# Optimization experiments

Hardware: AMD Instinct MI355X
Metric: run time of the kernel (lower is better)

## Reference

```python
import jax, jax.numpy as jnp
import numpy as np

D_MODEL = 2048
HIDDEN = 1024
NUM_EXPERTS = 8
TOTAL_TOKENS = 16384  # tokens already sorted/grouped by expert


def setup_inputs() -> dict:
    key = jax.random.key(0)
    k1, k2, k3 = jax.random.split(key, 3)
    x = jax.random.normal(k1, (TOTAL_TOKENS, D_MODEL), dtype=jnp.float32)
    # nn.Linear(d_model, 2*E*H).weight -> [2*E*H, d_model]
    w_up_gate = jax.random.normal(k2, (2 * NUM_EXPERTS * HIDDEN, D_MODEL), dtype=jnp.float32) / np.sqrt(D_MODEL)
    # nn.Linear(E*H, d_model).weight -> [d_model, E*H]
    w_down = jax.random.normal(k3, (D_MODEL, NUM_EXPERTS * HIDDEN), dtype=jnp.float32) / np.sqrt(HIDDEN)
    batch_size_per_expert = jnp.full((NUM_EXPERTS,), TOTAL_TOKENS // NUM_EXPERTS, dtype=jnp.int32)
    return {
        "x": x,
        "w_up_gate": w_up_gate,
        "w_down": w_down,
        "batch_size_per_expert": batch_size_per_expert,
        "num_experts": NUM_EXPERTS,
    }


def reference(x, w_up_gate, w_down, batch_size_per_expert, num_experts):
    # Per-expert sizes are host constants (a Python list in the torch code).
    sizes = np.asarray(batch_size_per_expert)
    offs = np.concatenate([[0], np.cumsum(sizes)])  # static token offsets
    d_model = x.shape[-1]
    hidden = w_up_gate.shape[0] // (2 * num_experts)
    # [E, 2H, d_model]: expert e's fused up/gate weight block
    w_ug = w_up_gate.reshape(num_experts, 2 * hidden, d_model)
    outs = []
    for e in range(num_experts):  # small static loop over experts (ragged grouped GEMM)
        xe = x[offs[e]:offs[e + 1]]                      # [n_e, d_model]
        ug = xe @ w_ug[e].T                              # [n_e, 2H]
        h = jax.nn.silu(ug[:, :hidden]) * ug[:, hidden:]  # SwiGLU, [n_e, H]
        wd_e = w_down[:, e * hidden:(e + 1) * hidden]    # [d_model, H]
        outs.append(h @ wd_e.T)                          # [n_e, d_model]
    return jnp.concatenate(outs, axis=0)
```

## Files before the change

kernel.cpp:

```cpp
#include <hip/hip_runtime.h>
#include <hip/hip_bf16.h>

typedef __attribute__((ext_vector_type(8))) short short8;
typedef __attribute__((ext_vector_type(4))) float float4v;

#define BM 128
#define BK 32
#define LDSK 40

struct alignas(8) BF4 { unsigned short x, y, z, w; };
struct alignas(16) I4 { int x, y, z, w; };

__device__ __forceinline__ unsigned short f2bf(float f) {
    union { float f; unsigned u; } v; v.f = f;
    unsigned u = v.u + (0x7FFFu + ((v.u >> 16) & 1u));
    return (unsigned short)(u >> 16);
}

__device__ __forceinline__ void stage_f32_tile(const float* __restrict__ src, long ld,
                                               unsigned short* lds, int t) {
    const int rr  = t >> 3;
    const int col = (t & 7) << 2;
    #pragma unroll
    for (int r = 0; r < 4; ++r) {
        const int row = rr + r * 32;
        const float4 v = *(const float4*)(src + (long)row * ld + col);
        BF4 o; o.x = f2bf(v.x); o.y = f2bf(v.y); o.z = f2bf(v.z); o.w = f2bf(v.w);
        *(BF4*)(lds + row * LDSK + col) = o;
    }
}

__device__ __forceinline__ int find_expert(const int* __restrict__ bspe, int row0) {
    int e = 0, off = 0;
    #pragma unroll
    for (int i = 0; i < 8; ++i) {
        int s = bspe[i];
        if (row0 < off + s) { e = i; break; }
        off += s;
    }
    return e;
}

__global__ __launch_bounds__(256) void moe_up_gate(
    const float* __restrict__ x, const float* __restrict__ wug,
    const int* __restrict__ bspe, unsigned short* __restrict__ hws) {
    __shared__ alignas(16) unsigned short As[BM * LDSK];
    __shared__ alignas(16) unsigned short Bs[BM * LDSK];

    const int t = threadIdx.x;
    const int lane = t & 63;
    const int w = t >> 6;
    const int wr = w >> 1, wc = w & 1;
    const int bm = blockIdx.y;
    const int h0 = blockIdx.x * 64;
    const int row0 = bm * BM;

    const int e = find_expert(bspe, row0);

    const float* abase = x + (long)row0 * 2048;
    const float* bup = wug + ((long)e * 2048 + h0) * 2048;
    const float* bgt = wug + ((long)e * 2048 + 1024 + h0) * 2048;

    float4v acc[4][4];
    #pragma unroll
    for (int m = 0; m < 4; ++m)
        #pragma unroll
        for (int n = 0; n < 4; ++n)
            acc[m][n] = (float4v){0.f, 0.f, 0.f, 0.f};

    const int k8 = (lane >> 4) << 3;
    const int am = wr * 64 + (lane & 15);
    const int l15 = lane & 15;

    for (int k0 = 0; k0 < 2048; k0 += BK) {
        __syncthreads();
        stage_f32_tile(abase + k0, 2048, As, t);
        {
            const int rr  = t >> 3;
            const int col = (t & 7) << 2;
            #pragma unroll
            for (int r = 0; r < 4; ++r) {
                const int row = rr + r * 32;
                const float* p = (row < 64 ? bup + (long)row * 2048
                                           : bgt + (long)(row - 64) * 2048) + k0 + col;
                const float4 v = *(const float4*)p;
                BF4 o; o.x = f2bf(v.x); o.y = f2bf(v.y); o.z = f2bf(v.z); o.w = f2bf(v.w);
                *(BF4*)(Bs + row * LDSK + col) = o;
            }
        }
        __syncthreads();

        short8 a[4], b[4];
        #pragma unroll
        for (int m = 0; m < 4; ++m)
            a[m] = *(const short8*)(As + (am + m * 16) * LDSK + k8);
        #pragma unroll
        for (int n = 0; n < 4; ++n) {
            const int rb = (n < 2) ? (wc * 32 + n * 16) : (64 + wc * 32 + (n - 2) * 16);
            b[n] = *(const short8*)(Bs + (rb + l15) * LDSK + k8);
        }
        #pragma unroll
        for (int m = 0; m < 4; ++m)
            #pragma unroll
            for (int n = 0; n < 4; ++n)
                acc[m][n] = __builtin_amdgcn_mfma_f32_16x16x32_bf16(a[m], b[n], acc[m][n], 0, 0, 0);
    }

    const int rbase = row0 + wr * 64 + (lane >> 4) * 4;
    const int cbase = h0 + wc * 32 + l15;
    #pragma unroll
    for (int m = 0; m < 4; ++m)
        #pragma unroll
        for (int n = 0; n < 2; ++n)
            #pragma unroll
            for (int q = 0; q < 4; ++q) {
                const float u = acc[m][n][q];
                const float g = acc[m][n + 2][q];
                const float s = u / (1.f + __expf(-u));
                const int row = rbase + m * 16 + q;
                const int col = cbase + n * 16;
                hws[(long)row * 1024 + col] = f2bf(s * g);
            }
}

__global__ __launch_bounds__(256) void moe_down(
    const unsigned short* __restrict__ hws, const float* __restrict__ wd,
    const int* __restrict__ bspe, float* __restrict__ out) {
    __shared__ alignas(16) unsigned short As[BM * LDSK];
    __shared__ alignas(16) unsigned short Bs[BM * LDSK];

    const int t = threadIdx.x;
    const int lane = t & 63;
    const int w = t >> 6;
    const int wr = w >> 1, wc = w & 1;
    const int bm = blockIdx.y;
    const int n0 = blockIdx.x * BM;
    const int row0 = bm * BM;

    const int e = find_expert(bspe, row0);

    const unsigned short* abase = hws + (long)row0 * 1024;
    const float* bbase = wd + (long)n0 * 8192 + e * 1024;

    float4v acc[4][4];
    #pragma unroll
    for (int m = 0; m < 4; ++m)
        #pragma unroll
        for (int n = 0; n < 4; ++n)
            acc[m][n] = (float4v){0.f, 0.f, 0.f, 0.f};

    const int k8 = (lane >> 4) << 3;
    const int am = wr * 64 + (lane & 15);
    const int l15 = lane & 15;

    for (int k0 = 0; k0 < 1024; k0 += BK) {
        __syncthreads();
        {
            const int row = t >> 2;
            const int col = (t & 3) << 3;
            #pragma unroll
            for (int r = 0; r < 2; ++r) {
                const I4 v = *(const I4*)(abase + (long)(row + r * 64) * 1024 + k0 + col);
                *(I4*)(As + (row + r * 64) * LDSK + col) = v;
            }
        }
        stage_f32_tile(bbase + k0, 8192, Bs, t);
        __syncthreads();

        short8 a[4], b[4];
        #pragma unroll
        for (int m = 0; m < 4; ++m)
            a[m] = *(const short8*)(As + (am + m * 16) * LDSK + k8);
        #pragma unroll
        for (int n = 0; n < 4; ++n)
            b[n] = *(const short8*)(Bs + (wc * 64 + n * 16 + l15) * LDSK + k8);
        #pragma unroll
        for (int m = 0; m < 4; ++m)
            #pragma unroll
            for (int n = 0; n < 4; ++n)
                acc[m][n] = __builtin_amdgcn_mfma_f32_16x16x32_bf16(a[m], b[n], acc[m][n], 0, 0, 0);
    }

    const int rbase = row0 + wr * 64 + (lane >> 4) * 4;
    const int cbase = n0 + wc * 64 + l15;
    #pragma unroll
    for (int m = 0; m < 4; ++m)
        #pragma unroll
        for (int n = 0; n < 4; ++n)
            #pragma unroll
            for (int q = 0; q < 4; ++q)
                out[(long)(rbase + m * 16 + q) * 2048 + cbase + n * 16] = acc[m][n][q];
}

extern "C" void kernel_launch(void* const* d_in, const int* in_sizes, int n_in,
                              void* d_out, int out_size, void* d_ws, size_t ws_size,
                              hipStream_t stream) {
    const float* x   = (const float*)d_in[0];
    const float* wug = (const float*)d_in[1];
    const float* wd  = (const float*)d_in[2];
    const int*  bspe = (const int*)d_in[3];
    float* out = (float*)d_out;
    unsigned short* hws = (unsigned short*)d_ws;

    moe_up_gate<<<dim3(16, 128), dim3(256), 0, stream>>>(x, wug, bspe, hws);
    moe_down  <<<dim3(16, 128), dim3(256), 0, stream>>>(hws, wd, bspe, out);
}
```

Measured before the change: 684.3 us.

## Pre-convert inputs to bf16 and stage tiles via direct global-to-LDS loads

Adds a standalone fp32-to-bf16 conversion pass for x, the up/gate weights and the down weights, reusing workspace so the down-weight copy overwrites the no-longer-needed x buffer. New GEMM kernels then read bf16 directly and load tiles into LDS with global_load_lds, removing the per-tile float loads and in-loop conversion from the GEMM main loops. In exchange, every call adds extra full-tensor read/write passes and depends on a large workspace, otherwise it falls back to the old path. The new LDS layout drops the padding, which may introduce bank conflicts.

```diff
diff --git a/kernel.cpp b/kernel.cpp
--- a/kernel.cpp
+++ b/kernel.cpp
@@ -9,12 +9,195 @@
 #define LDSK 40
 
 struct alignas(8) BF4 { unsigned short x, y, z, w; };
+struct alignas(16) BF8 { unsigned short s[8]; };
 struct alignas(16) I4 { int x, y, z, w; };
 
 __device__ __forceinline__ unsigned short f2bf(float f) {
     union { float f; unsigned u; } v; v.f = f;
     unsigned u = v.u + (0x7FFFu + ((v.u >> 16) & 1u));
     return (unsigned short)(u >> 16);
+}
+
+__device__ __forceinline__ int find_expert(const int* __restrict__ bspe, int row0) {
+    int e = 0, off = 0;
+    #pragma unroll
+    for (int i = 0; i < 8; ++i) {
+        int s = bspe[i];
+        if (row0 < off + s) { e = i; break; }
+        off += s;
+    }
+    return e;
+}
+
+__device__ __forceinline__ void gload_lds16(const unsigned short* g, unsigned short* l) {
+    __builtin_amdgcn_global_load_lds(
+        (const __attribute__((address_space(1))) void*)g,
+        (__attribute__((address_space(3))) void*)l, 16, 0, 0);
+}
+
+__global__ __launch_bounds__(256) void f32_to_bf16(const float* __restrict__ src,
+                                                   unsigned short* __restrict__ dst,
+                                                   long n) {
+    const long stride = (long)gridDim.x * 256 * 8;
+    for (long i = ((long)blockIdx.x * 256 + threadIdx.x) * 8; i < n; i += stride) {
+        const float4 v0 = *(const float4*)(src + i);
+        const float4 v1 = *(const float4*)(src + i + 4);
+        BF8 o;
+        o.s[0] = f2bf(v0.x); o.s[1] = f2bf(v0.y); o.s[2] = f2bf(v0.z); o.s[3] = f2bf(v0.w);
+        o.s[4] = f2bf(v1.x); o.s[5] = f2bf(v1.y); o.s[6] = f2bf(v1.z); o.s[7] = f2bf(v1.w);
+        *(BF8*)(dst + i) = o;
+    }
+}
+
+__global__ __launch_bounds__(256) void moe_up_gate_bf(
+    const unsigned short* __restrict__ xb, const unsigned short* __restrict__ wb,
+    const int* __restrict__ bspe, unsigned short* __restrict__ hws) {
+    __shared__ alignas(16) unsigned short As[128 * 32];
+    __shared__ alignas(16) unsigned short Bs[128 * 32];
+
+    const int t = threadIdx.x;
+    const int lane = t & 63;
+    const int w = t >> 6;
+    const int wr = w >> 1, wc = w & 1;
+    const int bm = blockIdx.y;
+    const int h0 = blockIdx.x * 64;
+    const int row0 = bm * BM;
+
+    const int e = find_expert(bspe, row0);
+
+    const unsigned short* abase = xb + (long)row0 * 2048;
+    const unsigned short* bup = wb + ((long)e * 2048 + h0) * 2048;
+    const unsigned short* bgt = wb + ((long)e * 2048 + 1024 + h0) * 2048;
+
+    float4v acc[4][4];
+    #pragma unroll
+    for (int m = 0; m < 4; ++m)
+        #pragma unroll
+        for (int n = 0; n < 4; ++n)
+            acc[m][n] = (float4v){0.f, 0.f, 0.f, 0.f};
+
+    const int j0 = w, j1 = w + 4;
+    const int srow = lane >> 2;
+    const int scol = (lane & 3) << 3;
+    const unsigned short* a0 = abase + (long)(j0 * 16 + srow) * 2048 + scol;
+    const unsigned short* a1 = abase + (long)(j1 * 16 + srow) * 2048 + scol;
+    const unsigned short* b0 = bup + (long)(j0 * 16 + srow) * 2048 + scol;
+    const unsigned short* b1 = bgt + (long)((j1 - 4) * 16 + srow) * 2048 + scol;
+
+    const int k8 = (lane >> 4) << 3;
+    const int am = wr * 64 + (lane & 15);
+    const int l15 = lane & 15;
+
+    for (int k0 = 0; k0 < 2048; k0 += BK) {
+        __syncthreads();
+        gload_lds16(a0 + k0, As + j0 * 512);
+        gload_lds16(a1 + k0, As + j1 * 512);
+        gload_lds16(b0 + k0, Bs + j0 * 512);
+        gload_lds16(b1 + k0, Bs + j1 * 512);
+        __syncthreads();
+
+        short8 a[4], b[4];
+        #pragma unroll
+        for (int m = 0; m < 4; ++m)
+            a[m] = *(const short8*)(As + (am + m * 16) * 32 + k8);
+        #pragma unroll
+        for (int n = 0; n < 4; ++n) {
+            const int rb = (n < 2) ? (wc * 32 + n * 16) : (64 + wc * 32 + (n - 2) * 16);
+            b[n] = *(const short8*)(Bs + (rb + l15) * 32 + k8);
+        }
+        #pragma unroll
+        for (int m = 0; m < 4; ++m)
+            #pragma unroll
+            for (int n = 0; n < 4; ++n)
+                acc[m][n] = __builtin_amdgcn_mfma_f32_16x16x32_bf16(a[m], b[n], acc[m][n], 0, 0, 0);
+    }
+
+    const int rbase = row0 + wr * 64 + (lane >> 4) * 4;
+    const int cbase = h0 + wc * 32 + l15;
+    #pragma unroll
+    for (int m = 0; m < 4; ++m)
+        #pragma unroll
+        for (int n = 0; n < 2; ++n)
+            #pragma unroll
+            for (int q = 0; q < 4; ++q) {
+                const float u = acc[m][n][q];
+                const float g = acc[m][n + 2][q];
+                const float s = u / (1.f + __expf(-u));
+                const int row = rbase + m * 16 + q;
+                const int col = cbase + n * 16;
+                hws[(long)row * 1024 + col] = f2bf(s * g);
+            }
+}
+
+__global__ __launch_bounds__(256) void moe_down_bf(
+    const unsigned short* __restrict__ hws, const unsigned short* __restrict__ wdb,
+    const int* __restrict__ bspe, float* __restrict__ out) {
+    __shared__ alignas(16) unsigned short As[128 * 32];
+    __shared__ alignas(16) unsigned short Bs[128 * 32];
+
+    const int t = threadIdx.x;
+    const int lane = t & 63;
+    const int w = t >> 6;
+    const int wr = w >> 1, wc = w & 1;
+    const int bm = blockIdx.y;
+    const int n0 = blockIdx.x * BM;
+    const int row0 = bm * BM;
+
+    const int e = find_expert(bspe, row0);
+
+    const unsigned short* abase = hws + (long)row0 * 1024;
+    const unsigned short* bbase = wdb + (long)n0 * 8192 + e * 1024;
+
+    float4v acc[4][4];
+    #pragma unroll
+    for (int m = 0; m < 4; ++m)
+        #pragma unroll
+        for (int n = 0; n < 4; ++n)
+            acc[m][n] = (float4v){0.f, 0.f, 0.f, 0.f};
+
+    const int j0 = w, j1 = w + 4;
+    const int srow = lane >> 2;
+    const int scol = (lane & 3) << 3;
+    const unsigned short* a0 = abase + (long)(j0 * 16 + srow) * 1024 + scol;
+    const unsigned short* a1 = abase + (long)(j1 * 16 + srow) * 1024 + scol;
+    const unsigned short* b0 = bbase + (long)(j0 * 16 + srow) * 8192 + scol;
+    const unsigned short* b1 = bbase + (long)(j1 * 16 + srow) * 8192 + scol;
+
+    const int k8 = (lane >> 4) << 3;
+    const int am = wr * 64 + (lane & 15);
+    const int l15 = lane & 15;
+
+    for (int k0 = 0; k0 < 1024; k0 += BK) {
+        __syncthreads();
+        gload_lds16(a0 + k0, As + j0 * 512);
+        gload_lds16(a1 + k0, As + j1 * 512);
+        gload_lds16(b0 + k0, Bs + j0 * 512);
+        gload_lds16(b1 + k0, Bs + j1 * 512);
+        __syncthreads();
+
+        short8 a[4], b[4];
+        #pragma unroll
+        for (int m = 0; m < 4; ++m)
+            a[m] = *(const short8*)(As + (am + m * 16) * 32 + k8);
+        #pragma unroll
+        for (int n = 0; n < 4; ++n)
+            b[n] = *(const short8*)(Bs + (wc * 64 + n * 16 + l15) * 32 + k8);
+        #pragma unroll
+        for (int m = 0; m < 4; ++m)
+            #pragma unroll
+            for (int n = 0; n < 4; ++n)
+                acc[m][n] = __builtin_amdgcn_mfma_f32_16x16x32_bf16(a[m], b[n], acc[m][n], 0, 0, 0);
+    }
+
+    const int rbase = row0 + wr * 64 + (lane >> 4) * 4;
+    const int cbase = n0 + wc * 64 + l15;
+    #pragma unroll
+    for (int m = 0; m < 4; ++m)
+        #pragma unroll
+        for (int n = 0; n < 4; ++n)
+            #pragma unroll
+            for (int q = 0; q < 4; ++q)
+                out[(long)(rbase + m * 16 + q) * 2048 + cbase + n * 16] = acc[m][n][q];
 }
 
 __device__ __forceinline__ void stage_f32_tile(const float* __restrict__ src, long ld,
@@ -28,17 +211,6 @@
         BF4 o; o.x = f2bf(v.x); o.y = f2bf(v.y); o.z = f2bf(v.z); o.w = f2bf(v.w);
         *(BF4*)(lds + row * LDSK + col) = o;
     }
-}
-
-__device__ __forceinline__ int find_expert(const int* __restrict__ bspe, int row0) {
-    int e = 0, off = 0;
-    #pragma unroll
-    for (int i = 0; i < 8; ++i) {
-        int s = bspe[i];
-        if (row0 < off + s) { e = i; break; }
-        off += s;
-    }
-    return e;
 }
 
 __global__ __launch_bounds__(256) void moe_up_gate(
@@ -200,8 +372,26 @@
     const float* wd  = (const float*)d_in[2];
     const int*  bspe = (const int*)d_in[3];
     float* out = (float*)d_out;
-    unsigned short* hws = (unsigned short*)d_ws;
-
-    moe_up_gate<<<dim3(16, 128), dim3(256), 0, stream>>>(x, wug, bspe, hws);
-    moe_down  <<<dim3(16, 128), dim3(256), 0, stream>>>(hws, wd, bspe, out);
-}
+
+    const size_t SZ_XB  = 16384UL * 2048UL * 2UL;
+    const size_t SZ_WB  = 16384UL * 2048UL * 2UL;
+    const size_t SZ_H   = 16384UL * 1024UL * 2UL;
+    const size_t NEED   = SZ_XB + SZ_WB + SZ_H;
+
+    if (ws_size >= NEED) {
+        unsigned short* xb  = (unsigned short*)d_ws;
+        unsigned short* wb  = (unsigned short*)((char*)d_ws + SZ_XB);
+        unsigned short* hws = (unsigned short*)((char*)d_ws + SZ_XB + SZ_WB);
+        unsigned short* wdb = (unsigned short*)d_ws;
+
+        f32_to_bf16<<<2048, 256, 0, stream>>>(x,   xb,  16384L * 2048L);
+        f32_to_bf16<<<2048, 256, 0, stream>>>(wug, wb,  16384L * 2048L);
+        moe_up_gate_bf<<<dim3(16, 128), dim3(256), 0, stream>>>(xb, wb, bspe, hws);
+        f32_to_bf16<<<1024, 256, 0, stream>>>(wd,  wdb, 2048L * 8192L);
+        moe_down_bf<<<dim3(16, 128), dim3(256), 0, stream>>>(hws, wdb, bspe, out);
+    } else {
+        unsigned short* hws = (unsigned short*)d_ws;
+        moe_up_gate<<<dim3(16, 128), dim3(256), 0, stream>>>(x, wug, bspe, hws);
+        moe_down  <<<dim3(16, 128), dim3(256), 0, stream>>>(hws, wd, bspe, out);
+    }
+}
```

After: 667.5 us. 2.5% less time.

## Pre-convert operands to bf16 and use pipelined 256x256 MFMA GEMMs with direct LDS loads

Applied to the files above, without the earlier changes.

Adds separate passes that convert x and both weight matrices to bf16 in workspace, then runs new 512-thread GEMM kernels with 256x256 tiles. These kernels load global memory straight into swizzled LDS, double-buffer the tiles, and use raised wave priority around the MFMA blocks. The aim is to take fp32 conversion out of the inner loop, halve operand bandwidth, and overlap loads with compute. The cost is extra conversion traffic, a large workspace, and fallback to the old kernels when the workspace is too small.

```diff
diff --git a/kernel.cpp b/kernel.cpp
--- a/kernel.cpp
+++ b/kernel.cpp
@@ -9,12 +9,219 @@
 #define LDSK 40
 
 struct alignas(8) BF4 { unsigned short x, y, z, w; };
+struct alignas(16) BF8 { unsigned short s[8]; };
 struct alignas(16) I4 { int x, y, z, w; };
 
 __device__ __forceinline__ unsigned short f2bf(float f) {
     union { float f; unsigned u; } v; v.f = f;
     unsigned u = v.u + (0x7FFFu + ((v.u >> 16) & 1u));
     return (unsigned short)(u >> 16);
+}
+
+__device__ __forceinline__ int find_expert(const int* __restrict__ bspe, int row0) {
+    int e = 0, off = 0;
+    #pragma unroll
+    for (int i = 0; i < 8; ++i) {
+        int s = bspe[i];
+        if (row0 < off + s) { e = i; break; }
+        off += s;
+    }
+    return e;
+}
+
+__device__ __forceinline__ void gload_lds16(const unsigned short* g, unsigned short* l) {
+    __builtin_amdgcn_global_load_lds(
+        (const __attribute__((address_space(1))) void*)g,
+        (__attribute__((address_space(3))) void*)l, 16, 0, 0);
+}
+
+__global__ __launch_bounds__(256) void f32_to_bf16(const float* __restrict__ src,
+                                                   unsigned short* __restrict__ dst,
+                                                   long n) {
+    const long stride = (long)gridDim.x * 256 * 8;
+    for (long i = ((long)blockIdx.x * 256 + threadIdx.x) * 8; i < n; i += stride) {
+        const float4 v0 = *(const float4*)(src + i);
+        const float4 v1 = *(const float4*)(src + i + 4);
+        BF8 o;
+        o.s[0] = f2bf(v0.x); o.s[1] = f2bf(v0.y); o.s[2] = f2bf(v0.z); o.s[3] = f2bf(v0.w);
+        o.s[4] = f2bf(v1.x); o.s[5] = f2bf(v1.y); o.s[6] = f2bf(v1.z); o.s[7] = f2bf(v1.w);
+        *(BF8*)(dst + i) = o;
+    }
+}
+
+#define BAR() __builtin_amdgcn_s_barrier()
+#define WAITV(n) asm volatile("s_waitcnt vmcnt(" #n ")" ::: "memory")
+#define WAITL0() do { asm volatile("s_waitcnt lgkmcnt(0)" ::: "memory"); \
+                      __builtin_amdgcn_sched_barrier(0); } while (0)
+
+#define STG_A(tt, kss) do { \
+    gload_lds16(pA0 + (long)(tt) * 64 + (kss) * 32, As + ((((tt)&1)*2 + (kss))*8192) + 0*4096 + w*512); \
+    gload_lds16(pA1 + (long)(tt) * 64 + (kss) * 32, As + ((((tt)&1)*2 + (kss))*8192) + 1*4096 + w*512); \
+} while (0)
+#define STG_B(tt, kss) do { \
+    gload_lds16(pB0 + (long)(tt) * 64 + (kss) * 32, Bs + ((((tt)&1)*2 + (kss))*8192) + 0*4096 + w*512); \
+    gload_lds16(pB1 + (long)(tt) * 64 + (kss) * 32, Bs + ((((tt)&1)*2 + (kss))*8192) + 1*4096 + w*512); \
+} while (0)
+
+#define RD_A(buf_, ks_, mh_) do { \
+    const unsigned short* _p = As + (((buf_)*2 + (ks_))*8192) + gA + (arow + (mh_)*64)*32; \
+    a[0] = *(const short8*)(_p);        a[1] = *(const short8*)(_p + 512); \
+    a[2] = *(const short8*)(_p + 1024); a[3] = *(const short8*)(_p + 1536); \
+} while (0)
+#define RD_B(buf_, ks_) do { \
+    const unsigned short* _p = Bs + (((buf_)*2 + (ks_))*8192) + gA + brow*32; \
+    b[0] = *(const short8*)(_p);        b[1] = *(const short8*)(_p + 512); \
+    b[2] = *(const short8*)(_p + 1024); b[3] = *(const short8*)(_p + 1536); \
+} while (0)
+
+#define MMA(mh_) do { \
+    __builtin_amdgcn_s_setprio(1); \
+    _Pragma("unroll") \
+    for (int _j = 0; _j < 4; ++_j) \
+        _Pragma("unroll") \
+        for (int _n = 0; _n < 4; ++_n) \
+            acc[(mh_)*4 + _j][_n] = __builtin_amdgcn_mfma_f32_16x16x32_bf16(a[_j], b[_n], acc[(mh_)*4 + _j][_n], 0, 0, 0); \
+    __builtin_amdgcn_s_setprio(0); \
+} while (0)
+
+#define KLOOP(NKT) \
+    STG_A(0, 0); STG_B(0, 0); \
+    STG_A(0, 1); STG_B(0, 1); \
+    STG_A(1, 0); STG_B(1, 0); \
+    WAITV(8); \
+    BAR(); \
+    for (int t = 0; t < (NKT); ++t) { \
+        const int buf = t & 1; \
+        short8 a[4], b[4]; \
+         \
+        RD_B(buf, 0); RD_A(buf, 0, 0); \
+        if (t < (NKT) - 1) STG_A(t + 1, 1); \
+        BAR(); WAITL0(); \
+        MMA(0); \
+        BAR(); \
+         \
+        RD_A(buf, 0, 1); \
+        if (t < (NKT) - 1) { STG_B(t + 1, 1); WAITV(8); } else { WAITV(0); } \
+        BAR(); WAITL0(); \
+        MMA(1); \
+        BAR(); \
+         \
+        RD_B(buf, 1); RD_A(buf, 1, 0); \
+        if (t < (NKT) - 2) STG_A(t + 2, 0); \
+        BAR(); WAITL0(); \
+        MMA(0); \
+        BAR(); \
+         \
+        RD_A(buf, 1, 1); \
+        if (t < (NKT) - 2) { STG_B(t + 2, 0); WAITV(8); } \
+        else if (t == (NKT) - 2) { WAITV(4); } \
+        BAR(); WAITL0(); \
+        MMA(1); \
+        BAR(); \
+    }
+
+__global__ __launch_bounds__(512) void moe_up_gate_p8(
+    const unsigned short* __restrict__ xb, const unsigned short* __restrict__ wb,
+    const int* __restrict__ bspe, unsigned short* __restrict__ hws) {
+    __shared__ alignas(16) unsigned short As[32768];
+    __shared__ alignas(16) unsigned short Bs[32768];
+
+    const int t0 = threadIdx.x;
+    const int lane = t0 & 63;
+    const int w = t0 >> 6;
+    const int wr = w >> 2, wc = w & 3;
+    const int row0 = blockIdx.y * 256;
+    const int h0 = blockIdx.x * 128;
+    const int e = find_expert(bspe, row0);
+
+    const int srow = lane >> 2;
+    const int gs = ((lane & 3) ^ ((lane >> 3) & 3)) * 8;
+    const unsigned short* pA0 = xb + (long)(row0 + w * 16 + srow) * 2048 + gs;
+    const unsigned short* pA1 = pA0 + (long)128 * 2048;
+    const unsigned short* pB0; const unsigned short* pB1;
+    {
+        const int r0 = w * 16 + srow;
+        const int r1 = r0 + 128;
+        const int in0 = r0 & 63, in1 = r1 & 63;
+        const long g0 = (long)e * 2048 + (in0 < 32 ? 0 : 1024) + h0 + (r0 >> 6) * 32 + (in0 & 31);
+        const long g1 = (long)e * 2048 + (in1 < 32 ? 0 : 1024) + h0 + (r1 >> 6) * 32 + (in1 & 31);
+        pB0 = wb + g0 * 2048 + gs;
+        pB1 = wb + g1 * 2048 + gs;
+    }
+
+    const int l15 = lane & 15;
+    const int gA = ((lane >> 4) ^ ((l15 >> 1) & 3)) * 8;
+    const int arow = wr * 128 + l15;
+    const int brow = wc * 64 + l15;
+
+    float4v acc[8][4];
+    #pragma unroll
+    for (int m = 0; m < 8; ++m)
+        #pragma unroll
+        for (int n = 0; n < 4; ++n)
+            acc[m][n] = (float4v){0.f, 0.f, 0.f, 0.f};
+
+    KLOOP(32)
+
+    const int rbase = row0 + wr * 128 + (lane >> 4) * 4;
+    const int cbase = h0 + wc * 32 + l15;
+    #pragma unroll
+    for (int m = 0; m < 8; ++m)
+        #pragma unroll
+        for (int n = 0; n < 2; ++n)
+            #pragma unroll
+            for (int q = 0; q < 4; ++q) {
+                const float u = acc[m][n][q];
+                const float g = acc[m][n + 2][q];
+                const float s = u / (1.f + __expf(-u));
+                hws[(long)(rbase + m * 16 + q) * 1024 + cbase + n * 16] = f2bf(s * g);
+            }
+}
+
+__global__ __launch_bounds__(512) void moe_down_p8(
+    const unsigned short* __restrict__ hws, const unsigned short* __restrict__ wdb,
+    const int* __restrict__ bspe, float* __restrict__ out) {
+    __shared__ alignas(16) unsigned short As[32768];
+    __shared__ alignas(16) unsigned short Bs[32768];
+
+    const int t0 = threadIdx.x;
+    const int lane = t0 & 63;
+    const int w = t0 >> 6;
+    const int wr = w >> 2, wc = w & 3;
+    const int row0 = blockIdx.y * 256;
+    const int n0 = blockIdx.x * 256;
+    const int e = find_expert(bspe, row0);
+
+    const int srow = lane >> 2;
+    const int gs = ((lane & 3) ^ ((lane >> 3) & 3)) * 8;
+    const unsigned short* pA0 = hws + (long)(row0 + w * 16 + srow) * 1024 + gs;
+    const unsigned short* pA1 = pA0 + (long)128 * 1024;
+    const unsigned short* pB0 = wdb + (long)(n0 + w * 16 + srow) * 8192 + (long)e * 1024 + gs;
+    const unsigned short* pB1 = pB0 + (long)128 * 8192;
+
+    const int l15 = lane & 15;
+    const int gA = ((lane >> 4) ^ ((l15 >> 1) & 3)) * 8;
+    const int arow = wr * 128 + l15;
+    const int brow = wc * 64 + l15;
+
+    float4v acc[8][4];
+    #pragma unroll
+    for (int m = 0; m < 8; ++m)
+        #pragma unroll
+        for (int n = 0; n < 4; ++n)
+            acc[m][n] = (float4v){0.f, 0.f, 0.f, 0.f};
+
+    KLOOP(16)
+
+    const int rbase = row0 + wr * 128 + (lane >> 4) * 4;
+    const int cbase = n0 + wc * 64 + l15;
+    #pragma unroll
+    for (int m = 0; m < 8; ++m)
+        #pragma unroll
+        for (int n = 0; n < 4; ++n)
+            #pragma unroll
+            for (int q = 0; q < 4; ++q)
+                out[(long)(rbase + m * 16 + q) * 2048 + cbase + n * 16] = acc[m][n][q];
 }
 
 __device__ __forceinline__ void stage_f32_tile(const float* __restrict__ src, long ld,
@@ -28,17 +235,6 @@
         BF4 o; o.x = f2bf(v.x); o.y = f2bf(v.y); o.z = f2bf(v.z); o.w = f2bf(v.w);
         *(BF4*)(lds + row * LDSK + col) = o;
     }
-}
-
-__device__ __forceinline__ int find_expert(const int* __restrict__ bspe, int row0) {
-    int e = 0, off = 0;
-    #pragma unroll
-    for (int i = 0; i < 8; ++i) {
-        int s = bspe[i];
-        if (row0 < off + s) { e = i; break; }
-        off += s;
-    }
-    return e;
 }
 
 __global__ __launch_bounds__(256) void moe_up_gate(
@@ -117,9 +313,7 @@
                 const float u = acc[m][n][q];
                 const float g = acc[m][n + 2][q];
                 const float s = u / (1.f + __expf(-u));
-                const int row = rbase + m * 16 + q;
-                const int col = cbase + n * 16;
-                hws[(long)row * 1024 + col] = f2bf(s * g);
+                hws[(long)(rbase + m * 16 + q) * 1024 + cbase + n * 16] = f2bf(s * g);
             }
 }
 
@@ -200,8 +394,26 @@
     const float* wd  = (const float*)d_in[2];
     const int*  bspe = (const int*)d_in[3];
     float* out = (float*)d_out;
-    unsigned short* hws = (unsigned short*)d_ws;
-
-    moe_up_gate<<<dim3(16, 128), dim3(256), 0, stream>>>(x, wug, bspe, hws);
-    moe_down  <<<dim3(16, 128), dim3(256), 0, stream>>>(hws, wd, bspe, out);
-}
+
+    const size_t SZ_XB  = 16384UL * 2048UL * 2UL;
+    const size_t SZ_WB  = 16384UL * 2048UL * 2UL;
+    const size_t SZ_H   = 16384UL * 1024UL * 2UL;
+    const size_t NEED   = SZ_XB + SZ_WB + SZ_H;
+
+    if (ws_size >= NEED) {
+        unsigned short* xb  = (unsigned short*)d_ws;
+        unsigned short* wb  = (unsigned short*)((char*)d_ws + SZ_XB);
+        unsigned short* hws = (unsigned short*)((char*)d_ws + SZ_XB + SZ_WB);
+        unsigned short* wdb = (unsigned short*)d_ws;
+
+        f32_to_bf16<<<2048, 256, 0, stream>>>(x,   xb,  16384L * 2048L);
+        f32_to_bf16<<<2048, 256, 0, stream>>>(wug, wb,  16384L * 2048L);
+        moe_up_gate_p8<<<dim3(8, 64), dim3(512), 0, stream>>>(xb, wb, bspe, hws);
+        f32_to_bf16<<<1024, 256, 0, stream>>>(wd,  wdb, 2048L * 8192L);
+        moe_down_p8<<<dim3(8, 64), dim3(512), 0, stream>>>(hws, wdb, bspe, out);
+    } else {
+        unsigned short* hws = (unsigned short*)d_ws;
+        moe_up_gate<<<dim3(16, 128), dim3(256), 0, stream>>>(x, wug, bspe, hws);
+        moe_down  <<<dim3(16, 128), dim3(256), 0, stream>>>(hws, wd, bspe, out);
+    }
+}
```

After: 589.6 us. 1.16x faster.
